# Optimization experiments

Measured on AMD Instinct MI355X. Metric: run time of the kernel, lower is better.

Reference implementation:

```python
import jax, jax.numpy as jnp
import numpy as np

H = 224          # image height (self.shape[0])
W_IMG = 224      # image width (self.shape[1])
CELLS = 7        # mask_generator num_cells
PAD = CELLS // 2 # reflect pad size
D = 512          # encoder feature dim
NUM_BATCHES = 30
BATCH = 100
EPS = 1e-8       # torch CosineSimilarity eps


def _encode(xb, Wenc):
    # stand-in encoder: 32x32 block average pool -> [B,3,7,7] -> linear to D
    B = xb.shape[0]
    feats = xb.reshape(B, 3, CELLS, H // CELLS, CELLS, W_IMG // CELLS).mean(axis=(3, 5))
    return feats.reshape(B, -1) @ Wenc  # [B, D]


def _cosine(a, b):
    # a: [1,D] (h_star), b: [B,D]; matches nn.CosineSimilarity(dim=1)
    num = jnp.sum(a * b, axis=1)
    den = jnp.maximum(jnp.linalg.norm(a, axis=1) * jnp.linalg.norm(b, axis=1), EPS)
    return num / den  # [B]


def _make_masks(grid, sx, sy):
    # grid: [B,1,7,7] binary floats; bilinear upsample, reflect pad, shifted crop
    B = grid.shape[0]
    up = jax.image.resize(grid, (B, 1, H, W_IMG), method='linear')
    padded = jnp.pad(up, ((0, 0), (0, 0), (PAD, PAD), (PAD, PAD)), mode='reflect')
    crop = jax.vmap(
        lambda g, i, j: jax.lax.dynamic_slice(g, (0, i, j), (1, H, W_IMG))
    )(padded, sx, sy)
    return crop  # [B,1,H,W]


def _relax(x, Wenc, grids, shifts_x, shifts_y):
    h_star = _encode(x, Wenc)  # [1, D]
    R0 = jnp.zeros((H, W_IMG), jnp.float32)
    U0 = jnp.zeros_like(R0)
    sow0 = jnp.full((H, W_IMG), 1e-10, jnp.float32)

    def sample_step(carry, inp):
        # sequential weighted running-mean / Welford variance update
        R, U, sow = carry
        s, m = inp  # s: scalar sim, m: [H,W] mask
        sow = sow + m
        R_new = R + m * (s - R) / sow
        U = U + (s - R_new) * (s - R) * m
        return (R_new, U, sow), None

    def batch_step(carry, binp):
        grid, sx, sy = binp
        masks = _make_masks(grid, sx, sy)        # [B,1,H,W]
        x_mask = x * masks                       # fill_vals_zeros=True path
        h = _encode(x_mask, Wenc)                # [B,D]
        sims = _cosine(h_star, h)                # [B]
        carry, _ = jax.lax.scan(sample_step, carry, (sims, masks[:, 0]))
        return carry, None

    (R, U, sow), _ = jax.lax.scan(batch_step, (R0, U0, sow0),
                                  (grids, shifts_x, shifts_y))
    uncertainty = U / (sow - 1.0)
    return jnp.stack([R, uncertainty])  # [2,H,W]: importance, uncertainty


def setup_inputs() -> dict:
    key = jax.random.key(0)
    k1, k2, k3, k4, k5 = jax.random.split(key, 5)
    x = jax.random.normal(k1, (1, 3, H, W_IMG), jnp.float32)
    Wenc = jax.random.normal(k2, (3 * CELLS * CELLS, D), jnp.float32) * 0.05
    grids = (jax.random.uniform(k3, (NUM_BATCHES, BATCH, 1, CELLS, CELLS)) < 0.5).astype(jnp.float32)
    shifts_x = jax.random.randint(k4, (NUM_BATCHES, BATCH), 0, CELLS)
    shifts_y = jax.random.randint(k5, (NUM_BATCHES, BATCH), 0, CELLS)
    return {"x": x, "Wenc": Wenc, "grids": grids,
            "shifts_x": shifts_x, "shifts_y": shifts_y}


def reference(x, Wenc, grids, shifts_x, shifts_y):
    return _relax(x, Wenc, grids, shifts_x, shifts_y)
```

## Files before the change

### kernel.cpp

```cpp
#include <hip/hip_runtime.h>
#include <math.h>

#define NS 3000
#define NF 147
#define ND 512
#define NSIG 49
#define NSAMP 4
#define NHBLK 750
#define NBLK_VT 1029
#define TROW 52

#define OFF_WT     0
#define OFF_FEATS  6272
#define OFF_T      236928
#define OFF_G      611584

__device__ __forceinline__ void wt_compute(int sigma, int p, int& i0c, int& i1c,
                                           float& w0, float& w1) {
  int k = p + sigma - 3;
  int r = k < 0 ? -k : (k > 223 ? 446 - k : k);
  float tc = (float)(2 * r - 31) * (1.0f / 64.0f);
  float fl = floorf(tc);
  int i0 = (int)fl;
  float fr = tc - fl;
  i0c = min(max(i0, 0), 6);
  i1c = min(max(i0 + 1, 0), 6);
  w0 = 1.0f - fr;
  w1 = fr;
}

__global__ void __launch_bounds__(256) k_VT(const float* __restrict__ x,
                                            float* __restrict__ ws) {
  __shared__ __align__(16) float sX[32][36];
  __shared__ __align__(16) float sVt[7][36];
  __shared__ __align__(16) float sWXd[7][36];
  __shared__ __align__(16) float sWYd[7][7][36];
  __shared__ float red[4];

  int b = blockIdx.x;
  int t = threadIdx.x;
  if (b >= NBLK_VT) {
    if (b == NBLK_VT) {
      float4* WT = (float4*)(ws + OFF_WT);
      for (int e = t; e < 7 * 224; e += 256) {
        int sigma = e / 224, p = e % 224;
        int i0c, i1c; float w0, w1;
        wt_compute(sigma, p, i0c, i1c, w0, w1);
        WT[e] = make_float4(w0, w1, __int_as_float(i0c), __int_as_float(i1c));
      }
    } else {
      int e = (b - NBLK_VT - 1) * 256 + t;
      if (e < 3 * 2401) ws[OFF_G + e] = 0.f;
    }
    return;
  }

  int f = b % NF;
  int sy = b / NF;
  int c = f / 49, rem = f % 49, cy = rem / 7, cx = rem % 7;

  const float* xb = x + (c * 224 + cy * 32) * 224 + cx * 32;
  float psum = 0.f;
  for (int idx = t; idx < 1024; idx += 256) {
    int yy = idx >> 5, xx = idx & 31;
    float v = xb[yy * 224 + xx];
    sX[yy][xx] = v;
    psum += v;
  }

  if (t < 224) {
    int gx = t >> 5, x0 = t & 31;
    int i0, i1; float w0, w1;
    wt_compute(sy, cx * 32 + x0, i0, i1, w0, w1);
    sWXd[gx][x0] = (gx == i0 ? w0 : 0.f) + (gx == i1 ? w1 : 0.f);
  }
  for (int e = t; e < 7 * 7 * 32; e += 256) {
    int sx = e / 224, r2 = e % 224, gy = r2 >> 5, y0 = r2 & 31;
    int i0, i1; float w0, w1;
    wt_compute(sx, cy * 32 + y0, i0, i1, w0, w1);
    sWYd[sx][gy][y0] = (gy == i0 ? w0 : 0.f) + (gy == i1 ? w1 : 0.f);
  }

  if (sy == 0) {
    float acc = psum;
    for (int off = 32; off; off >>= 1) acc += __shfl_down(acc, off);
    int wave = t >> 6, lane = t & 63;
    if (lane == 0) red[wave] = acc;
  }
  __syncthreads();
  if (sy == 0 && t == 0)
    ws[OFF_FEATS + f] = (red[0] + red[1] + red[2] + red[3]) * (1.0f / 1024.0f);

  if (t < 224) {
    int y0 = t / 7, gx = t % 7;
    const float4* wrow = (const float4*)sWXd[gx];
    const float4* xrow = (const float4*)sX[y0];
    float acc = 0.f;
    #pragma unroll
    for (int x4 = 0; x4 < 8; ++x4) {
      float4 w = wrow[x4], v = xrow[x4];
      acc = fmaf(w.x, v.x, fmaf(w.y, v.y, fmaf(w.z, v.z, fmaf(w.w, v.w, acc))));
    }
    sVt[gx][y0] = acc;
  }
  __syncthreads();

  for (int e = t; e < 343; e += 256) {
    int sx = e / 49, r2 = e % 49, gy = r2 / 7, gx = r2 % 7;
    const float4* wrow = (const float4*)sWYd[sx][gy];
    const float4* vrow = (const float4*)sVt[gx];
    float acc = 0.f;
    #pragma unroll
    for (int y4 = 0; y4 < 8; ++y4) {
      float w = 0.f;
      float4 w4 = wrow[y4], v4 = vrow[y4];
      (void)w;
      acc = fmaf(w4.x, v4.x, fmaf(w4.y, v4.y, fmaf(w4.z, v4.z, fmaf(w4.w, v4.w, acc))));
    }
    ws[OFF_T + ((sx * 7 + sy) * NF + f) * TROW + gy * 7 + gx] = acc * (1.0f / 1024.0f);
  }
  if (t < 21) {
    int sx = t / 3, pd = 49 + t % 3;
    ws[OFF_T + ((sx * 7 + sy) * NF + f) * TROW + pd] = 0.f;
  }
}

__global__ void __launch_bounds__(256) k_H2s(const float* __restrict__ Wenc,
                                             const float* __restrict__ grids,
                                             const int* __restrict__ shx,
                                             const int* __restrict__ shy,
                                             float* __restrict__ ws) {
  __shared__ __align__(16) float sF[NF * NSAMP];
  __shared__ __align__(16) float sGr[NSAMP][56];
  __shared__ float sFeat[NF];
  __shared__ int   sSig[NSAMP];
  __shared__ float sRed[2][NSAMP][4];
  __shared__ float sRedH[4];
  __shared__ float sS[NSAMP];
  int t = threadIdx.x;
  int b = blockIdx.x;
  int i0s = b * NSAMP;
  for (int e = t; e < NSAMP * 49; e += 256) sGr[e / 49][e % 49] = grids[i0s * 49 + e];
  if (t < NSAMP * 7) sGr[t / 7][49 + t % 7] = 0.f;
  if (t < NSAMP) sSig[t] = shx[i0s + t] * 7 + shy[i0s + t];
  if (t < NF) sFeat[t] = ws[OFF_FEATS + t];
  __syncthreads();
  for (int idx = t; idx < NF * NSAMP; idx += 256) {
    int r = idx / NF, f = idx - r * NF;
    const float4* T2 = (const float4*)(ws + OFF_T + (sSig[r] * NF + f) * TROW);
    const float4* gr = (const float4*)sGr[r];
    float acc = 0.f;
    #pragma unroll
    for (int g4 = 0; g4 < 13; ++g4) {
      float4 a = T2[g4], g = gr[g4];
      acc = fmaf(a.x, g.x, fmaf(a.y, g.y, fmaf(a.z, g.z, fmaf(a.w, g.w, acc))));
    }
    sF[f * NSAMP + r] = acc;
  }
  __syncthreads();
  float accA[NSAMP], accB[NSAMP];
  #pragma unroll
  for (int r = 0; r < NSAMP; ++r) { accA[r] = 0.f; accB[r] = 0.f; }
  float h0 = 0.f, h1 = 0.f;
  const float2* W2 = (const float2*)Wenc;
  const float4* sF4 = (const float4*)sF;
  for (int f = 0; f < NF; ++f) {
    float2 w = W2[f * (ND / 2) + t];
    float fe = sFeat[f];
    h0 = fmaf(fe, w.x, h0);
    h1 = fmaf(fe, w.y, h1);
    float4 a4 = sF4[f];
    float a[NSAMP] = {a4.x, a4.y, a4.z, a4.w};
    #pragma unroll
    for (int r = 0; r < NSAMP; ++r) {
      accA[r] = fmaf(a[r], w.x, accA[r]);
      accB[r] = fmaf(a[r], w.y, accB[r]);
    }
  }
  int wave = t >> 6, lane = t & 63;
  float hq = h0 * h0 + h1 * h1;
  for (int off = 32; off; off >>= 1) hq += __shfl_down(hq, off);
  if (lane == 0) sRedH[wave] = hq;
  #pragma unroll
  for (int r = 0; r < NSAMP; ++r) {
    float np = accA[r] * h0 + accB[r] * h1;
    float sp = accA[r] * accA[r] + accB[r] * accB[r];
    for (int off = 32; off; off >>= 1) {
      np += __shfl_down(np, off);
      sp += __shfl_down(sp, off);
    }
    if (lane == 0) { sRed[0][r][wave] = np; sRed[1][r][wave] = sp; }
  }
  __syncthreads();
  if (t == 0) sRedH[0] = sqrtf(sRedH[0] + sRedH[1] + sRedH[2] + sRedH[3]);
  __syncthreads();
  if (t < NSAMP) {
    float np = sRed[0][t][0] + sRed[0][t][1] + sRed[0][t][2] + sRed[0][t][3];
    float sp = sRed[1][t][0] + sRed[1][t][1] + sRed[1][t][2] + sRed[1][t][3];
    float den = fmaxf(sRedH[0] * sqrtf(sp), 1e-8f);
    sS[t] = np / den;
  }
  __syncthreads();
  for (int e = t; e < NSAMP * 3 * 49; e += 256) {
    int k = e % 49;
    int rp = e / 49;
    int r = rp / 3, p = rp - r * 3;
    float gv = sGr[r][k];
    if (gv != 0.f) {
      float s = sS[r];
      float add = (p == 0) ? 1.f : ((p == 1) ? s : s * s);
      atomicAdd(&ws[OFF_G + p * 2401 + sSig[r] * 49 + k], add);
    }
  }
}

__global__ void __launch_bounds__(256) k_CO(const float* __restrict__ ws,
                                            float* __restrict__ out) {
  __shared__ float Gl[3 * 2401];
  __shared__ float sC[NF];
  int b = blockIdx.x;
  int t = threadIdx.x;
  for (int e = t; e < 3 * 2401; e += 256) Gl[e] = ws[OFF_G + e];
  __syncthreads();
  const float4* WT = (const float4*)(ws + OFF_WT);
  if (t < NF) {
    int k = t / 49, r = t - k * 49;
    int sx = r / 7, gy = r % 7;
    float acc = 0.f;
    for (int sy = 0; sy < 7; ++sy) {
      float4 wt = WT[sy * 224 + b];
      int i0 = __float_as_int(wt.z), i1 = __float_as_int(wt.w);
      int base = k * 2401 + (sx * 7 + sy) * 49 + gy * 7;
      acc += wt.x * Gl[base + i0] + wt.y * Gl[base + i1];
    }
    sC[t] = acc;
  }
  __syncthreads();
  if (t < 224) {
    int py = t;
    float S0 = 0.f, S1 = 0.f, S2 = 0.f;
    for (int sx = 0; sx < 7; ++sx) {
      float4 wt = WT[sx * 224 + py];
      int i0 = __float_as_int(wt.z), i1 = __float_as_int(wt.w);
      int base = sx * 7;
      S0 += wt.x * sC[base + i0]      + wt.y * sC[base + i1];
      S1 += wt.x * sC[49 + base + i0] + wt.y * sC[49 + base + i1];
      S2 += wt.x * sC[98 + base + i0] + wt.y * sC[98 + base + i1];
    }
    float W = 1e-10f + S0;
    float R = S1 / W;
    float U = S2 - S1 * S1 / W;
    out[py * 224 + b] = R;
    out[224 * 224 + py * 224 + b] = U / (W - 1.0f);
  }
}

extern "C" void kernel_launch(void* const* d_in, const int* in_sizes, int n_in,
                              void* d_out, int out_size, void* d_ws, size_t ws_size,
                              hipStream_t stream) {
  const float* x     = (const float*)d_in[0];
  const float* Wenc  = (const float*)d_in[1];
  const float* grids = (const float*)d_in[2];
  const int*   shx   = (const int*)d_in[3];
  const int*   shy   = (const int*)d_in[4];
  float* out = (float*)d_out;
  float* ws  = (float*)d_ws;

  k_VT<<<NBLK_VT + 30, 256, 0, stream>>>(x, ws);
  k_H2s<<<NHBLK, 256, 0, stream>>>(Wenc, grids, shx, shy, ws);
  k_CO<<<224, 256, 0, stream>>>(ws, out);
}
```

Measured before the change: 98.53 us.

## Sort samples by shift and merge per-block atomic accumulation into G

Adds an extra block to the first kernel that counting-sorts the 3000 samples by their shift index into a workspace order array. The encoder kernel then processes 6 samples per block in sorted order, and when every sample in a block shares the same shift it sums their contributions in registers before issuing one atomic per cell instead of one per sample. The goal is to cut global atomic contention and the number of blocks. The cost is a serial prefix scan in one block, indirect gathers of grids, and a wider shared-memory stride. Floating-point summation order changes.

```diff
diff --git a/kernel.cpp b/kernel.cpp
--- a/kernel.cpp
+++ b/kernel.cpp
@@ -5,8 +5,8 @@
 #define NF 147
 #define ND 512
 #define NSIG 49
-#define NSAMP 4
-#define NHBLK 750
+#define NSAMP 6
+#define NHBLK 500
 #define NBLK_VT 1029
 #define TROW 52
 
@@ -14,6 +14,7 @@
 #define OFF_FEATS  6272
 #define OFF_T      236928
 #define OFF_G      611584
+#define OFF_ORD    618880
 
 __device__ __forceinline__ void wt_compute(int sigma, int p, int& i0c, int& i1c,
                                            float& w0, float& w1) {
@@ -30,12 +31,15 @@
 }
 
 __global__ void __launch_bounds__(256) k_VT(const float* __restrict__ x,
+                                            const int* __restrict__ shx,
+                                            const int* __restrict__ shy,
                                             float* __restrict__ ws) {
   __shared__ __align__(16) float sX[32][36];
   __shared__ __align__(16) float sVt[7][36];
   __shared__ __align__(16) float sWXd[7][36];
   __shared__ __align__(16) float sWYd[7][7][36];
   __shared__ float red[4];
+  __shared__ int hist[64];
 
   int b = blockIdx.x;
   int t = threadIdx.x;
@@ -48,9 +52,25 @@
         wt_compute(sigma, p, i0c, i1c, w0, w1);
         WT[e] = make_float4(w0, w1, __int_as_float(i0c), __int_as_float(i1c));
       }
-    } else {
+    } else if (b <= NBLK_VT + 29) {
       int e = (b - NBLK_VT - 1) * 256 + t;
       if (e < 3 * 2401) ws[OFF_G + e] = 0.f;
+    } else {
+      if (t < 49) hist[t] = 0;
+      __syncthreads();
+      for (int i = t; i < NS; i += 256)
+        atomicAdd(&hist[shx[i] * 7 + shy[i]], 1);
+      __syncthreads();
+      if (t == 0) {
+        int run = 0;
+        for (int s2 = 0; s2 < 49; ++s2) { int c2 = hist[s2]; hist[s2] = run; run += c2; }
+      }
+      __syncthreads();
+      int* ord = (int*)ws + OFF_ORD;
+      for (int i = t; i < NS; i += 256) {
+        int s2 = shx[i] * 7 + shy[i];
+        ord[atomicAdd(&hist[s2], 1)] = i;
+      }
     }
     return;
   }
@@ -112,9 +132,7 @@
     float acc = 0.f;
     #pragma unroll
     for (int y4 = 0; y4 < 8; ++y4) {
-      float w = 0.f;
       float4 w4 = wrow[y4], v4 = vrow[y4];
-      (void)w;
       acc = fmaf(w4.x, v4.x, fmaf(w4.y, v4.y, fmaf(w4.z, v4.z, fmaf(w4.w, v4.w, acc))));
     }
     ws[OFF_T + ((sx * 7 + sy) * NF + f) * TROW + gy * 7 + gx] = acc * (1.0f / 1024.0f);
@@ -130,20 +148,33 @@
                                              const int* __restrict__ shx,
                                              const int* __restrict__ shy,
                                              float* __restrict__ ws) {
-  __shared__ __align__(16) float sF[NF * NSAMP];
+  __shared__ __align__(16) float sF[NF * 8];
   __shared__ __align__(16) float sGr[NSAMP][56];
   __shared__ float sFeat[NF];
   __shared__ int   sSig[NSAMP];
+  __shared__ int   sId[NSAMP];
   __shared__ float sRed[2][NSAMP][4];
   __shared__ float sRedH[4];
   __shared__ float sS[NSAMP];
+  __shared__ int   sUni;
   int t = threadIdx.x;
   int b = blockIdx.x;
   int i0s = b * NSAMP;
-  for (int e = t; e < NSAMP * 49; e += 256) sGr[e / 49][e % 49] = grids[i0s * 49 + e];
+  const int* ord = (const int*)ws + OFF_ORD;
+  if (t < NSAMP) {
+    int id = ord[i0s + t];
+    sId[t] = id;
+    sSig[t] = shx[id] * 7 + shy[id];
+  }
+  if (t < NF) sFeat[t] = ws[OFF_FEATS + t];
+  if (t == 0) sUni = 1;
+  __syncthreads();
+  for (int e = t; e < NSAMP * 49; e += 256) {
+    int r = e / 49, k = e % 49;
+    sGr[r][k] = grids[sId[r] * 49 + k];
+  }
   if (t < NSAMP * 7) sGr[t / 7][49 + t % 7] = 0.f;
-  if (t < NSAMP) sSig[t] = shx[i0s + t] * 7 + shy[i0s + t];
-  if (t < NF) sFeat[t] = ws[OFF_FEATS + t];
+  if (t < NSAMP && t > 0 && sSig[t] != sSig[0]) sUni = 0;
   __syncthreads();
   for (int idx = t; idx < NF * NSAMP; idx += 256) {
     int r = idx / NF, f = idx - r * NF;
@@ -155,8 +186,9 @@
       float4 a = T2[g4], g = gr[g4];
       acc = fmaf(a.x, g.x, fmaf(a.y, g.y, fmaf(a.z, g.z, fmaf(a.w, g.w, acc))));
     }
-    sF[f * NSAMP + r] = acc;
-  }
+    sF[f * 8 + r] = acc;
+  }
+  if (t < NF * 2) sF[(t / 2) * 8 + 6 + (t & 1)] = 0.f;
   __syncthreads();
   float accA[NSAMP], accB[NSAMP];
   #pragma unroll
@@ -169,8 +201,9 @@
     float fe = sFeat[f];
     h0 = fmaf(fe, w.x, h0);
     h1 = fmaf(fe, w.y, h1);
-    float4 a4 = sF4[f];
-    float a[NSAMP] = {a4.x, a4.y, a4.z, a4.w};
+    float4 a4 = sF4[2 * f];
+    float4 b4 = sF4[2 * f + 1];
+    float a[NSAMP] = {a4.x, a4.y, a4.z, a4.w, b4.x, b4.y};
     #pragma unroll
     for (int r = 0; r < NSAMP; ++r) {
       accA[r] = fmaf(a[r], w.x, accA[r]);
@@ -201,15 +234,30 @@
     sS[t] = np / den;
   }
   __syncthreads();
-  for (int e = t; e < NSAMP * 3 * 49; e += 256) {
-    int k = e % 49;
-    int rp = e / 49;
-    int r = rp / 3, p = rp - r * 3;
-    float gv = sGr[r][k];
-    if (gv != 0.f) {
-      float s = sS[r];
-      float add = (p == 0) ? 1.f : ((p == 1) ? s : s * s);
-      atomicAdd(&ws[OFF_G + p * 2401 + sSig[r] * 49 + k], add);
+  if (sUni) {
+    for (int e = t; e < 3 * 49; e += 256) {
+      int k = e % 49, p = e / 49;
+      float acc = 0.f;
+      #pragma unroll
+      for (int r = 0; r < NSAMP; ++r) {
+        float gv = sGr[r][k];
+        float s = sS[r];
+        float add = (p == 0) ? 1.f : ((p == 1) ? s : s * s);
+        acc += (gv != 0.f) ? add : 0.f;
+      }
+      if (acc != 0.f) atomicAdd(&ws[OFF_G + p * 2401 + sSig[0] * 49 + k], acc);
+    }
+  } else {
+    for (int e = t; e < NSAMP * 3 * 49; e += 256) {
+      int k = e % 49;
+      int rp = e / 49;
+      int r = rp / 3, p = rp - r * 3;
+      float gv = sGr[r][k];
+      if (gv != 0.f) {
+        float s = sS[r];
+        float add = (p == 0) ? 1.f : ((p == 1) ? s : s * s);
+        atomicAdd(&ws[OFF_G + p * 2401 + sSig[r] * 49 + k], add);
+      }
     }
   }
 }
@@ -266,7 +314,7 @@
   float* out = (float*)d_out;
   float* ws  = (float*)d_ws;
 
-  k_VT<<<NBLK_VT + 30, 256, 0, stream>>>(x, ws);
+  k_VT<<<NBLK_VT + 31, 256, 0, stream>>>(x, shx, shy, ws);
   k_H2s<<<NHBLK, 256, 0, stream>>>(Wenc, grids, shx, shy, ws);
   k_CO<<<224, 256, 0, stream>>>(ws, out);
 }
```

Result: no change. 96.88 us, median of 2 (-1.7%).
